# Kernel tuning notes

Hardware: AMD Instinct MI355X
Metric: run time of the kernel (lower is better)

Reference implementation:

```python
import jax, jax.numpy as jnp
import numpy as np

ALPHABET = 26

def _shift(position, S):
    if position == 0:
        return jnp.zeros(S, dtype=jnp.int32)
    elif position == 1:
        return jnp.arange(S, dtype=jnp.int32) % ALPHABET
    elif position == 2:
        return jnp.arange(S, dtype=jnp.int32) // 26 + 1 % 26  # faithful to torch precedence: +1
    elif position == 3:
        return jnp.arange(S, dtype=jnp.int32) // 676 + 1 % 26
    raise ValueError('Invalid rotor position')


def setup_inputs() -> dict:
    key = jax.random.key(0)
    k1, k2 = jax.random.split(key)
    B, S = 128, 8192
    signalInput = jax.random.normal(k1, (B, S, ALPHABET), dtype=jnp.float32)
    # xavier_normal_ on a 26x26 matrix: std = sqrt(2/(26+26))
    std = float(np.sqrt(2.0 / (ALPHABET + ALPHABET)))
    rotor = jax.random.normal(k2, (ALPHABET, ALPHABET), dtype=jnp.float32) * std
    return {"signalInput": signalInput, "rotor": rotor}


def reference(signalInput, rotor):
    position = 1
    B, S, _ = signalInput.shape
    # L2-normalize rotor rows (torch.norm(dim=1, keepdim=True))
    rn = rotor / jnp.linalg.norm(rotor, axis=1, keepdims=True)  # [26,26]
    shift = _shift(position, S)                                  # [S]
    # one_hot((i + shift[s]) % 26) @ rn  ==  gather rn rows
    idx = (jnp.arange(ALPHABET, dtype=jnp.int32)[None, :] + shift[:, None]) % ALPHABET  # [S,26]
    M = rn[idx]                                                  # [S,26,26]
    # per-token 1x26 @ 26x26 bmm, batch-independent rotation matrix
    out = jnp.einsum('bsi,sij->bsj', signalInput, M)             # [B,S,26]
    return jax.nn.softmax(out, axis=2)
```

## Files before the change

kernel.cpp:

```cpp
#include <hip/hip_runtime.h>
#include <math.h>

#define ALPHA 26
#define ROW_PAD 32
#define TPB 256
#define TILE_FLOATS (TPB * ALPHA)

typedef __attribute__((address_space(3))) float lds_f;
typedef const __attribute__((address_space(1))) float glb_f;

__global__ void rotor_norm_kernel(const float* __restrict__ rotor,
                                  float* __restrict__ rn) {
    int i = threadIdx.x;
    if (i < ALPHA) {
        float ss = 0.f;
        #pragma unroll
        for (int j = 0; j < ALPHA; ++j) {
            float v = rotor[i * ALPHA + j];
            ss += v * v;
        }
        float inv = 1.0f / sqrtf(ss);
        #pragma unroll
        for (int j = 0; j < ALPHA; ++j)
            rn[i * ROW_PAD + j] = rotor[i * ALPHA + j] * inv;
    }
}

__global__ __launch_bounds__(TPB) void rotor_main(
        const float* __restrict__ x,
        const float* __restrict__ rn,
        float* __restrict__ out) {
    __shared__ float tile[TILE_FLOATS];

    const int tid = threadIdx.x;
    const int wave = tid >> 6;
    const long long blockTok = (long long)blockIdx.x * TPB;
    const float* gin = x + blockTok * ALPHA;
    float* gout = out + blockTok * ALPHA;

    #pragma unroll
    for (int it = 0; it < 6; ++it) {
        int v4 = it * TPB + tid;
        __builtin_amdgcn_global_load_lds(
            (glb_f*)(gin + v4 * 4),
            (lds_f*)&tile[(it * TPB + wave * 64) * 4],
            16, 0, 0);
    }
    if (tid < 128) {
        int v4 = 6 * TPB + tid;
        __builtin_amdgcn_global_load_lds(
            (glb_f*)(gin + v4 * 4),
            (lds_f*)&tile[(6 * TPB + wave * 64) * 4],
            16, 0, 0);
    }
    __syncthreads();

    const int n = (int)blockTok + tid;
    const int r = (n & 8191) % 26;
    int shift = 26 - r; if (shift == 26) shift = 0;

    const float* myx = &tile[tid * ALPHA];
    float xv[ALPHA];
    #pragma unroll
    for (int k = 0; k < ALPHA; ++k) {
        int idx = k + shift;
        idx = (idx >= ALPHA) ? idx - ALPHA : idx;
        xv[k] = myx[idx];
    }

    float acc[ALPHA];
    #pragma unroll
    for (int j = 0; j < ALPHA; ++j) acc[j] = 0.f;

    #pragma unroll
    for (int k = 0; k < ALPHA; ++k) {
        const float xk = xv[k];
        #pragma unroll
        for (int j = 0; j < ALPHA; ++j)
            acc[j] = fmaf(xk, rn[k * ROW_PAD + j], acc[j]);
    }

    float m = acc[0];
    #pragma unroll
    for (int j = 1; j < ALPHA; ++j) m = fmaxf(m, acc[j]);
    float sum = 0.f;
    #pragma unroll
    for (int j = 0; j < ALPHA; ++j) { acc[j] = __expf(acc[j] - m); sum += acc[j]; }
    float inv = 1.0f / sum;
    #pragma unroll
    for (int j = 0; j < ALPHA; ++j) acc[j] *= inv;

    __syncthreads();
    #pragma unroll
    for (int j = 0; j < ALPHA; ++j)
        tile[tid * ALPHA + j] = acc[j];
    __syncthreads();

    #pragma unroll
    for (int it = 0; it < 6; ++it) {
        int v4 = it * TPB + tid;
        float4 d = *(const float4*)&tile[v4 * 4];
        *(float4*)(gout + v4 * 4) = d;
    }
    if (tid < 128) {
        int v4 = 6 * TPB + tid;
        float4 d = *(const float4*)&tile[v4 * 4];
        *(float4*)(gout + v4 * 4) = d;
    }
}

extern "C" void kernel_launch(void* const* d_in, const int* in_sizes, int n_in,
                              void* d_out, int out_size, void* d_ws, size_t ws_size,
                              hipStream_t stream) {
    const float* x     = (const float*)d_in[0];
    const float* rotor = (const float*)d_in[1];
    float* out = (float*)d_out;
    float* rn  = (float*)d_ws;

    rotor_norm_kernel<<<1, 64, 0, stream>>>(rotor, rn);

    const int tokens = out_size / ALPHA;
    const int blocks = tokens / TPB;
    rotor_main<<<blocks, TPB, 0, stream>>>(x, rn, out);
}
```

Before: 204.5 us.

## Make LDS staging wave-local to drop block barriers and raise occupancy hint

Reorganizes the LDS staging so each wave loads and stores only the 64 tokens it computes, which lets the kernel replace the three block-wide __syncthreads with a per-wave vmcnt wait. The 26-float tail per wave is handled with a float2 load and store instead of a tid<128 branch. It also adds a min-blocks-per-CU hint to launch_bounds, which constrains register allocation. The aim is to let waves in a block progress independently instead of stalling at barriers. The risk is correctness if cross-lane LDS visibility inside a wave depends on the missing lgkmcnt waits, and register pressure from the launch-bounds hint could cause spills.

```diff
diff --git a/kernel.cpp b/kernel.cpp
--- a/kernel.cpp
+++ b/kernel.cpp
@@ -4,7 +4,6 @@
 #define ALPHA 26
 #define ROW_PAD 32
 #define TPB 256
-#define TILE_FLOATS (TPB * ALPHA)
 
 typedef __attribute__((address_space(3))) float lds_f;
 typedef const __attribute__((address_space(1))) float glb_f;
@@ -26,36 +25,35 @@
     }
 }
 
-__global__ __launch_bounds__(TPB) void rotor_main(
+__global__ __launch_bounds__(TPB, 6) void rotor_main(
         const float* __restrict__ x,
         const float* __restrict__ rn,
         float* __restrict__ out) {
-    __shared__ float tile[TILE_FLOATS];
+    __shared__ float tile[TPB * ALPHA];
 
-    const int tid = threadIdx.x;
+    const int tid  = threadIdx.x;
+    const int lane = tid & 63;
     const int wave = tid >> 6;
-    const long long blockTok = (long long)blockIdx.x * TPB;
-    const float* gin = x + blockTok * ALPHA;
-    float* gout = out + blockTok * ALPHA;
+
+    const long long blockF = (long long)blockIdx.x * (TPB * ALPHA);
+    const int waveF = wave * (64 * ALPHA);
+    const float* gin  = x   + blockF;
+    float*       gout = out + blockF;
 
     #pragma unroll
     for (int it = 0; it < 6; ++it) {
-        int v4 = it * TPB + tid;
         __builtin_amdgcn_global_load_lds(
-            (glb_f*)(gin + v4 * 4),
-            (lds_f*)&tile[(it * TPB + wave * 64) * 4],
+            (glb_f*)(gin + waveF + it * 256 + lane * 4),
+            (lds_f*)&tile[waveF + it * 256],
             16, 0, 0);
     }
-    if (tid < 128) {
-        int v4 = 6 * TPB + tid;
-        __builtin_amdgcn_global_load_lds(
-            (glb_f*)(gin + v4 * 4),
-            (lds_f*)&tile[(6 * TPB + wave * 64) * 4],
-            16, 0, 0);
+    {
+        float2 d = *(const float2*)(gin + waveF + 1536 + lane * 2);
+        *(float2*)&tile[waveF + 1536 + lane * 2] = d;
     }
-    __syncthreads();
+    asm volatile("s_waitcnt vmcnt(0)" ::: "memory");
 
-    const int n = (int)blockTok + tid;
+    const int n = blockIdx.x * TPB + tid;
     const int r = (n & 8191) % 26;
     int shift = 26 - r; if (shift == 26) shift = 0;
 
@@ -90,22 +88,18 @@
     #pragma unroll
     for (int j = 0; j < ALPHA; ++j) acc[j] *= inv;
 
-    __syncthreads();
     #pragma unroll
     for (int j = 0; j < ALPHA; ++j)
         tile[tid * ALPHA + j] = acc[j];
-    __syncthreads();
 
     #pragma unroll
     for (int it = 0; it < 6; ++it) {
-        int v4 = it * TPB + tid;
-        float4 d = *(const float4*)&tile[v4 * 4];
-        *(float4*)(gout + v4 * 4) = d;
+        float4 d = *(const float4*)&tile[waveF + it * 256 + lane * 4];
+        *(float4*)(gout + waveF + it * 256 + lane * 4) = d;
     }
-    if (tid < 128) {
-        int v4 = 6 * TPB + tid;
-        float4 d = *(const float4*)&tile[v4 * 4];
-        *(float4*)(gout + v4 * 4) = d;
+    {
+        float2 d = *(const float2*)&tile[waveF + 1536 + lane * 2];
+        *(float2*)(gout + waveF + 1536 + lane * 2) = d;
     }
 }
 
```

Result: no change. 203.0 us (-0.8%).
